# Optimization experiments

Measured on AMD Instinct MI355X. Metric: run time of the kernel, lower is better.

The kernel has to match this reference:

```python
import jax, jax.numpy as jnp
import numpy as np

N_HEADS = 8
D_K = 256
SCALE = D_K ** -0.5


def setup_inputs() -> dict:
    key = jax.random.key(0)
    k1, k2, k3 = jax.random.split(key, 3)
    B, C, H, W = 8, 256, 32, 32
    x = jax.random.normal(k1, (B, C, H, W), dtype=jnp.float32)
    Wp = jax.random.normal(k2, (C, N_HEADS * D_K * 3), dtype=jnp.float32) * (C ** -0.5)
    bp = jnp.zeros((N_HEADS * D_K * 3,), dtype=jnp.float32)
    Wo = jax.random.normal(k3, (N_HEADS * D_K, C), dtype=jnp.float32) * ((N_HEADS * D_K) ** -0.5)
    bo = jnp.zeros((C,), dtype=jnp.float32)
    return {"x": x, "Wp": Wp, "bp": bp, "Wo": Wo, "bo": bo}


def reference(x, Wp, bp, Wo, bo):
    B, C, H, W = x.shape
    S = H * W
    # [B,C,H,W] -> [B,S,C] tokens
    xt = x.reshape(B, C, S).transpose(0, 2, 1)
    qkv = (xt @ Wp + bp).reshape(B, S, N_HEADS, 3 * D_K)
    q, k, v = jnp.split(qkv, 3, axis=-1)  # each [B,S,H,dk]
    attn = jnp.einsum('bihd,bjhd->bijh', q, k) * SCALE
    attn = jax.nn.softmax(attn, axis=2)  # over j (keys)
    res = jnp.einsum('bijh,bjhd->bihd', attn, v).reshape(B, S, N_HEADS * D_K)
    res = res @ Wo + bo + xt  # residual
    return res.transpose(0, 2, 1).reshape(B, C, H, W)
```

## Files before the change

kernel.cpp:

```cpp
#include <hip/hip_runtime.h>

#define NH    8
#define DK    256
#define SS    1024
#define QSCALE 0.09016844136947155f
#define TSH   8192

using frag8  = __attribute__((ext_vector_type(8))) short;
using f32x16 = __attribute__((ext_vector_type(16))) float;

__device__ __forceinline__ unsigned short f2bf(float f) {
    unsigned int u = __float_as_uint(f);
    return (unsigned short)((u + 0x7FFFu + ((u >> 16) & 1u)) >> 16);
}
__device__ __forceinline__ unsigned int pk2bf(float lo, float hi) {
    unsigned int ul = __float_as_uint(lo), uh = __float_as_uint(hi);
    ul += 0x7FFFu + ((ul >> 16) & 1u);
    uh += 0x7FFFu + ((uh >> 16) & 1u);
    return (ul >> 16) | (uh & 0xFFFF0000u);
}

__device__ __forceinline__ void load_lds16(const void* g, void* l) {
    __builtin_amdgcn_global_load_lds(
        (const __attribute__((address_space(1))) unsigned int*)g,
        (__attribute__((address_space(3))) unsigned int*)l, 16, 0, 0);
}


__global__ __launch_bounds__(256) void k0_all(
    const float* __restrict__ x,  unsigned short* __restrict__ xbT,
    const float* __restrict__ Wp, unsigned short* __restrict__ WptT,
    const float* __restrict__ Wo, unsigned short* __restrict__ WotT)
{
    __shared__ float tile[32][33];
    const int bid = blockIdx.x;
    const float* in; unsigned short* outp; int C, c0, r0; size_t pbase; int psz;
    if (bid < 2048) {
        int rr = bid;
        int b = rr >> 8;
        in = x + (size_t)b * 256 * 1024;
        C = 1024; c0 = (rr & 31) * 32; r0 = ((rr >> 5) & 7) * 32;
        psz = 8192; pbase = (size_t)(b * 32 + (c0 >> 5)); outp = xbT;
    } else if (bid < 3584) {
        int rr = bid - 2048;
        in = Wp; C = 6144; c0 = (rr % 192) * 32; r0 = (rr / 192) * 32;
        psz = 8192; pbase = (size_t)(c0 >> 5); outp = WptT;
    } else {
        int rr = bid - 3584;
        in = Wo; C = 256; c0 = (rr & 7) * 32; r0 = (rr >> 3) * 32;
        psz = 65536; pbase = (size_t)(c0 >> 5); outp = WotT;
    }
    const int tx = threadIdx.x & 31, ty = threadIdx.x >> 5;
#pragma unroll
    for (int j = 0; j < 4; j++)
        tile[ty + j * 8][tx] = in[(size_t)(r0 + ty + j * 8) * C + c0 + tx];
    __syncthreads();
    const int k = r0 + tx;
    unsigned short* dst = outp + pbase * psz + ((k >> 3) * 32) * 8 + (k & 7);
#pragma unroll
    for (int j = 0; j < 4; j++)
        dst[(ty + j * 8) * 8] = f2bf(tile[tx][ty + j * 8]);
}

__global__ __launch_bounds__(256) void k1_qkv(
    const unsigned short* __restrict__ xbT, const unsigned short* __restrict__ WptT,
    const float* __restrict__ bp,
    unsigned short* __restrict__ qb, unsigned short* __restrict__ kb,
    unsigned short* __restrict__ vb)
{
    __shared__ unsigned short Xs[2][4096];
    __shared__ unsigned short Ws[2][4096];
    const int t = threadIdx.x;
    const int wave = t >> 6, lane = t & 63;
    const int l32 = lane & 31, hw = lane >> 5;
    const int n0 = blockIdx.x * 128, m0 = blockIdx.y * 128;
    const int b = m0 >> 10, s0 = m0 & 1023;

    const int h = n0 / 768;
    const int rem = n0 - h * 768;
    const int tt = rem >> 8;
    const int dcol0 = rem & 255;

    const unsigned short* Xg = xbT + (size_t)(b * 32 + (s0 >> 5)) * TSH;
    const unsigned short* Wg = WptT + (size_t)(n0 >> 5) * TSH;

    f32x16 acc[4];
#pragma unroll
    for (int j = 0; j < 4; j++)
#pragma unroll
        for (int r = 0; r < 16; r++) acc[j][r] = 0.f;

    auto stage = [&](int buf, int kt) {
#pragma unroll
        for (int j = 0; j < 4; j++) {
            int rgn = wave * 4 + j;
            if (rgn < 8) {
                int p = rgn >> 1, half = rgn & 1;
                load_lds16(Xg + (size_t)p * TSH + kt * 1024 + half * 512 + lane * 8,
                           &Xs[buf][p * 1024 + half * 512]);
            } else {
                int r2 = rgn - 8, p = r2 >> 1, half = r2 & 1;
                load_lds16(Wg + (size_t)p * TSH + kt * 1024 + half * 512 + lane * 8,
                           &Ws[buf][p * 1024 + half * 512]);
            }
        }
    };

    stage(0, 0);
    __syncthreads();

    for (int kt = 0; kt < 8; kt++) {
        const int cur = kt & 1;
        if (kt < 7) stage(cur ^ 1, kt + 1);
        const unsigned short* Fa = (tt < 2) ? &Ws[cur][wave * 1024] : &Xs[cur][wave * 1024];
        const unsigned short* Fb = (tt < 2) ? &Xs[cur][0] : &Ws[cur][0];
#pragma unroll
        for (int t2 = 0; t2 < 2; t2++) {
            frag8 af = *(const frag8*)(Fa + (2 * t2 + hw) * 256 + l32 * 8);
#pragma unroll
            for (int j = 0; j < 4; j++) {
                frag8 bf = *(const frag8*)(Fb + j * 1024 + (2 * t2 + hw) * 256 + l32 * 8);
                acc[j] = __builtin_amdgcn_mfma_f32_32x32x16_bf16(af, bf, acc[j], 0, 0, 0);
            }
        }
        __syncthreads();
    }

    if (tt < 2) {
        const float sc = (tt == 0) ? QSCALE : 1.0f;
        unsigned short* dst0 = (tt == 0 ? qb : kb);
        const int dc0 = (dcol0 + wave * 32) >> 3;
#pragma unroll
        for (int G = 0; G < 4; G++) {
            float4 bb = *(const float4*)(&bp[n0 + wave * 32 + 4 * hw + 8 * G]);
#pragma unroll
            for (int j = 0; j < 4; j++) {
                unsigned short* cell = dst0
                    + (size_t)((b * NH + h) * 32 + (s0 >> 5) + j) * TSH
                    + ((dc0 + G) * 32 + l32) * 8 + 4 * hw;
                uint2 st;
                st.x = pk2bf((acc[j][4 * G + 0] + bb.x) * sc, (acc[j][4 * G + 1] + bb.y) * sc);
                st.y = pk2bf((acc[j][4 * G + 2] + bb.z) * sc, (acc[j][4 * G + 3] + bb.w) * sc);
                *(uint2*)cell = st;
            }
        }
    } else {
        unsigned short* vt = vb + (size_t)((b * NH + h) * 32 + (s0 >> 5) + wave) * TSH;
#pragma unroll
        for (int j = 0; j < 4; j++) {
            const int d = dcol0 + j * 32 + l32;
            const float bv = bp[n0 + j * 32 + l32];
#pragma unroll
            for (int G = 0; G < 4; G++) {
                int g = G >> 1;
                unsigned short* cell = vt + (g * 2 + hw) * 2048 + d * 8 + 4 * (G & 1);
                uint2 st;
                st.x = pk2bf(acc[j][4 * G + 0] + bv, acc[j][4 * G + 1] + bv);
                st.y = pk2bf(acc[j][4 * G + 2] + bv, acc[j][4 * G + 3] + bv);
                *(uint2*)cell = st;
            }
        }
    }
}

__global__ __launch_bounds__(256, 2) void k2_attn(
    const unsigned short* __restrict__ qb, const unsigned short* __restrict__ kb,
    const unsigned short* __restrict__ vb, unsigned short* __restrict__ ob)
{
    __shared__ unsigned short Ks[2][TSH];
    __shared__ unsigned short Vs[2][TSH];

    const int t = threadIdx.x;
    const int wave = t >> 6, lane = t & 63;
    const int l32 = lane & 31, hw = lane >> 5;

    const int flat = blockIdx.x;
    const int xcd = flat & 7, tt2 = flat >> 3;
    const int qt = tt2 & 7;
    const int bh = xcd * 8 + (tt2 >> 3);

    frag8 qf[16];
    {
        const unsigned short* qp = qb + ((size_t)bh * 32 + qt * 4 + wave) * TSH
                                 + hw * 256 + l32 * 8;
#pragma unroll
        for (int s = 0; s < 16; s++) qf[s] = *(const frag8*)(qp + s * 512);
    }

    f32x16 acc[8];
#pragma unroll
    for (int nb = 0; nb < 8; nb++)
#pragma unroll
        for (int r = 0; r < 16; r++) acc[nb][r] = 0.f;
    float lsum = 0.f;

    const unsigned short* kt0 = kb + (size_t)bh * 32 * TSH;
    const unsigned short* vt0 = vb + (size_t)bh * 32 * TSH;

#pragma unroll
    for (int j = 0; j < 4; j++) {
        int c = wave * 4 + j;
        load_lds16(kt0 + c * 512 + lane * 8, &Ks[0][c * 512]);
        load_lds16(vt0 + c * 512 + lane * 8, &Vs[0][c * 512]);
    }
    __syncthreads();

    for (int kt = 0; kt < 32; kt++) {
        const int cur = kt & 1;

        if (kt < 31) {
            const unsigned short* kg = kt0 + (size_t)(kt + 1) * TSH;
            const unsigned short* vg = vt0 + (size_t)(kt + 1) * TSH;
#pragma unroll
            for (int j = 0; j < 4; j++) {
                int c = wave * 4 + j;
                load_lds16(kg + c * 512 + lane * 8, &Ks[cur ^ 1][c * 512]);
                load_lds16(vg + c * 512 + lane * 8, &Vs[cur ^ 1][c * 512]);
            }
        }

        f32x16 sa0, sa1;
#pragma unroll
        for (int r = 0; r < 16; r++) { sa0[r] = 0.f; sa1[r] = 0.f; }
#pragma unroll
        for (int s = 0; s < 16; s += 2) {
            frag8 kf0 = *(const frag8*)(&Ks[cur][(2 * s + hw) * 256 + l32 * 8]);
            frag8 kf1 = *(const frag8*)(&Ks[cur][(2 * s + 2 + hw) * 256 + l32 * 8]);
            sa0 = __builtin_amdgcn_mfma_f32_32x32x16_bf16(kf0, qf[s], sa0, 0, 0, 0);
            sa1 = __builtin_amdgcn_mfma_f32_32x32x16_bf16(kf1, qf[s + 1], sa1, 0, 0, 0);
        }

        float p[16];
#pragma unroll
        for (int e = 0; e < 16; e++) {
            p[e] = exp2f(sa0[e] + sa1[e]);
            lsum += p[e];
        }
        frag8 pf[2];
#pragma unroll
        for (int g = 0; g < 2; g++) {
            uint4 w;
            w.x = pk2bf(p[g * 8 + 0], p[g * 8 + 1]);
            w.y = pk2bf(p[g * 8 + 2], p[g * 8 + 3]);
            w.z = pk2bf(p[g * 8 + 4], p[g * 8 + 5]);
            w.w = pk2bf(p[g * 8 + 6], p[g * 8 + 7]);
            pf[g] = *(frag8*)&w;
        }

#pragma unroll
        for (int g = 0; g < 2; g++)
#pragma unroll
            for (int nb = 0; nb < 8; nb++) {
                frag8 vf = *(const frag8*)(&Vs[cur][(g * 2 + hw) * 2048 + (nb * 32 + l32) * 8]);
                acc[nb] = __builtin_amdgcn_mfma_f32_32x32x16_bf16(vf, pf[g], acc[nb], 0, 0, 0);
            }

        __syncthreads();
    }

    lsum += __shfl_xor(lsum, 32);
    const float li = 1.f / lsum;

    unsigned short* opan = ob + ((size_t)bh * 32 + qt * 4 + wave) * TSH;
#pragma unroll
    for (int nb = 0; nb < 8; nb++)
#pragma unroll
        for (int G = 0; G < 4; G++) {
            unsigned short* cell = opan + ((nb * 4 + G) * 32 + l32) * 8 + 4 * hw;
            uint2 st;
            st.x = pk2bf(acc[nb][4 * G + 0] * li, acc[nb][4 * G + 1] * li);
            st.y = pk2bf(acc[nb][4 * G + 2] * li, acc[nb][4 * G + 3] * li);
            *(uint2*)cell = st;
        }
}

__global__ __launch_bounds__(256) void k3_proj(
    const unsigned short* __restrict__ Ob, const unsigned short* __restrict__ WotT,
    const float* __restrict__ bo, const float* __restrict__ x,
    float* __restrict__ out)
{
    __shared__ unsigned short As[2][2048];
    __shared__ unsigned short Bs[2][4096];
    const int t = threadIdx.x;
    const int wave = t >> 6, lane = t & 63;
    const int l32 = lane & 31, hw = lane >> 5;
    const int wc = wave & 1, wt = wave >> 1;
    const int c0 = blockIdx.x * 64, m0 = blockIdx.y * 128;
    const int b = m0 >> 10, s0 = m0 & 1023;

    const unsigned short* Ag = WotT + (size_t)(c0 >> 5) * 65536;

    f32x16 acc[2];
#pragma unroll
    for (int pp = 0; pp < 2; pp++)
#pragma unroll
        for (int r = 0; r < 16; r++) acc[pp][r] = 0.f;

    auto stage = [&](int buf, int kt) {
        const int hh = kt >> 3, lc = (kt & 7) * 4;
#pragma unroll
        for (int j = 0; j < 3; j++) {
            int rgn = wave * 3 + j;
            if (rgn < 4) {
                int wp = rgn >> 1, half = rgn & 1;
                load_lds16(Ag + (size_t)wp * 65536 + kt * 1024 + half * 512 + lane * 8,
                           &As[buf][wp * 1024 + half * 512]);
            } else {
                int r2 = rgn - 4, p = r2 >> 1, half = r2 & 1;
                load_lds16(Ob + (size_t)((b * NH + hh) * 32 + (s0 >> 5) + p) * TSH
                               + lc * 256 + half * 512 + lane * 8,
                           &Bs[buf][p * 1024 + half * 512]);
            }
        }
    };

    stage(0, 0);
    __syncthreads();

    for (int kt = 0; kt < 64; kt++) {
        const int cur = kt & 1;
        if (kt < 63) stage(cur ^ 1, kt + 1);
#pragma unroll
        for (int t2 = 0; t2 < 2; t2++) {
            frag8 af = *(const frag8*)(&As[cur][wc * 1024 + (2 * t2 + hw) * 256 + l32 * 8]);
#pragma unroll
            for (int pp = 0; pp < 2; pp++) {
                frag8 bf = *(const frag8*)(&Bs[cur][(wt * 2 + pp) * 1024 + (2 * t2 + hw) * 256 + l32 * 8]);
                acc[pp] = __builtin_amdgcn_mfma_f32_32x32x16_bf16(af, bf, acc[pp], 0, 0, 0);
            }
        }
        __syncthreads();
    }

#pragma unroll
    for (int G = 0; G < 4; G++) {
        float4 bb = *(const float4*)(&bo[c0 + wc * 32 + 4 * hw + 8 * G]);
#pragma unroll
        for (int pp = 0; pp < 2; pp++) {
            const int s = s0 + wt * 64 + pp * 32 + l32;
#pragma unroll
            for (int e = 0; e < 4; e++) {
                const int ch = c0 + wc * 32 + 4 * hw + 8 * G + e;
                const float bbe = (e == 0) ? bb.x : (e == 1) ? bb.y : (e == 2) ? bb.z : bb.w;
                size_t off = (size_t)(b * 256 + ch) * 1024 + s;
                out[off] = acc[pp][4 * G + e] + bbe + x[off];
            }
        }
    }
}

extern "C" void kernel_launch(void* const* d_in, const int* in_sizes, int n_in,
                              void* d_out, int out_size, void* d_ws, size_t ws_size,
                              hipStream_t stream)
{
    const float* x  = (const float*)d_in[0];
    const float* Wp = (const float*)d_in[1];
    const float* bp = (const float*)d_in[2];
    const float* Wo = (const float*)d_in[3];
    const float* bo = (const float*)d_in[4];
    float* out = (float*)d_out;

    char* ws = (char*)d_ws;
    unsigned short* qb   = (unsigned short*)(ws);
    unsigned short* kb   = (unsigned short*)(ws + 33554432);
    unsigned short* vb   = (unsigned short*)(ws + 67108864);
    unsigned short* xbT  = (unsigned short*)(ws + 100663296);
    unsigned short* WptT = (unsigned short*)(ws + 104857600);
    unsigned short* WotT = (unsigned short*)(ws + 108003328);

    k0_all<<<dim3(4096), 256, 0, stream>>>(x, xbT, Wp, WptT, Wo, WotT);
    k1_qkv<<<dim3(48, 64), 256, 0, stream>>>(xbT, WptT, bp, qb, kb, vb);
    k2_attn<<<dim3(512), 256, 0, stream>>>(qb, kb, vb, qb );
    k3_proj<<<dim3(4, 64), 256, 0, stream>>>(qb, WotT, bo, x, out);
}
```

Baseline: 225.3 us.

## Enlarge QKV and projection GEMM tiles and unroll double-buffer loops statically

The QKV GEMM now computes 256x128 tiles per block (8 accumulators per wave), which halves the grid and raises reuse of the weight tile. The attention and QKV main loops are unrolled by two so LDS buffer indices become compile-time constants, removing dynamic buffer selection. The output projection moves to 512-thread blocks with a K-step of 64, giving each wave one accumulator and half as many loop iterations and barriers. In exchange, register pressure in the QKV kernel and LDS use per block go up, and the smaller QKV grid means fewer blocks to spread across CUs.

After: 229.6 us. About the same (+1.9%).

```diff
diff --git a/kernel.cpp b/kernel.cpp
--- a/kernel.cpp
+++ b/kernel.cpp
@@ -68,12 +68,13 @@
     unsigned short* __restrict__ qb, unsigned short* __restrict__ kb,
     unsigned short* __restrict__ vb)
 {
-    __shared__ unsigned short Xs[2][4096];
+    __shared__ unsigned short Xs[2][8192];
     __shared__ unsigned short Ws[2][4096];
     const int t = threadIdx.x;
     const int wave = t >> 6, lane = t & 63;
     const int l32 = lane & 31, hw = lane >> 5;
-    const int n0 = blockIdx.x * 128, m0 = blockIdx.y * 128;
+    const int n0 = blockIdx.x * 128;
+    const int m0 = blockIdx.y * 256;
     const int b = m0 >> 10, s0 = m0 & 1023;
 
     const int h = n0 / 768;
@@ -84,47 +85,65 @@
     const unsigned short* Xg = xbT + (size_t)(b * 32 + (s0 >> 5)) * TSH;
     const unsigned short* Wg = WptT + (size_t)(n0 >> 5) * TSH;
 
-    f32x16 acc[4];
-#pragma unroll
-    for (int j = 0; j < 4; j++)
+    f32x16 acc[8];
+#pragma unroll
+    for (int j = 0; j < 8; j++)
 #pragma unroll
         for (int r = 0; r < 16; r++) acc[j][r] = 0.f;
 
     auto stage = [&](int buf, int kt) {
 #pragma unroll
-        for (int j = 0; j < 4; j++) {
-            int rgn = wave * 4 + j;
-            if (rgn < 8) {
+        for (int j = 0; j < 6; j++) {
+            int rgn = wave * 6 + j;
+            if (rgn < 16) {
                 int p = rgn >> 1, half = rgn & 1;
                 load_lds16(Xg + (size_t)p * TSH + kt * 1024 + half * 512 + lane * 8,
                            &Xs[buf][p * 1024 + half * 512]);
             } else {
-                int r2 = rgn - 8, p = r2 >> 1, half = r2 & 1;
+                int r2 = rgn - 16, p = r2 >> 1, half = r2 & 1;
                 load_lds16(Wg + (size_t)p * TSH + kt * 1024 + half * 512 + lane * 8,
                            &Ws[buf][p * 1024 + half * 512]);
             }
         }
     };
 
+    auto body = [&](const unsigned short* Xb, const unsigned short* Wb) {
+        if (tt < 2) {
+#pragma unroll
+            for (int t2 = 0; t2 < 2; t2++) {
+                frag8 af = *(const frag8*)(Wb + wave * 1024 + (2 * t2 + hw) * 256 + l32 * 8);
+#pragma unroll
+                for (int j = 0; j < 8; j++) {
+                    frag8 bf = *(const frag8*)(Xb + j * 1024 + (2 * t2 + hw) * 256 + l32 * 8);
+                    acc[j] = __builtin_amdgcn_mfma_f32_32x32x16_bf16(af, bf, acc[j], 0, 0, 0);
+                }
+            }
+        } else {
+#pragma unroll
+            for (int t2 = 0; t2 < 2; t2++) {
+                frag8 bfv[4];
+#pragma unroll
+                for (int j = 0; j < 4; j++)
+                    bfv[j] = *(const frag8*)(Wb + j * 1024 + (2 * t2 + hw) * 256 + l32 * 8);
+#pragma unroll
+                for (int mi = 0; mi < 2; mi++) {
+                    frag8 af = *(const frag8*)(Xb + (wave * 2 + mi) * 1024 + (2 * t2 + hw) * 256 + l32 * 8);
+#pragma unroll
+                    for (int j = 0; j < 4; j++)
+                        acc[mi * 4 + j] = __builtin_amdgcn_mfma_f32_32x32x16_bf16(af, bfv[j], acc[mi * 4 + j], 0, 0, 0);
+                }
+            }
+        }
+    };
+
     stage(0, 0);
     __syncthreads();
-
-    for (int kt = 0; kt < 8; kt++) {
-        const int cur = kt & 1;
-        if (kt < 7) stage(cur ^ 1, kt + 1);
-        const unsigned short* Fa = (tt < 2) ? &Ws[cur][wave * 1024] : &Xs[cur][wave * 1024];
-        const unsigned short* Fb = (tt < 2) ? &Xs[cur][0] : &Ws[cur][0];
-#pragma unroll
-        for (int t2 = 0; t2 < 2; t2++) {
-            frag8 af = *(const frag8*)(Fa + (2 * t2 + hw) * 256 + l32 * 8);
-#pragma unroll
-            for (int j = 0; j < 4; j++) {
-                frag8 bf = *(const frag8*)(Fb + j * 1024 + (2 * t2 + hw) * 256 + l32 * 8);
-                acc[j] = __builtin_amdgcn_mfma_f32_32x32x16_bf16(af, bf, acc[j], 0, 0, 0);
-            }
-        }
-        __syncthreads();
-    }
+    for (int kt = 0; kt < 6; kt += 2) {
+        stage(1, kt + 1); body(&Xs[0][0], &Ws[0][0]); __syncthreads();
+        stage(0, kt + 2); body(&Xs[1][0], &Ws[1][0]); __syncthreads();
+    }
+    stage(1, 7); body(&Xs[0][0], &Ws[0][0]); __syncthreads();
+    body(&Xs[1][0], &Ws[1][0]);
 
     if (tt < 2) {
         const float sc = (tt == 0) ? QSCALE : 1.0f;
@@ -134,7 +153,7 @@
         for (int G = 0; G < 4; G++) {
             float4 bb = *(const float4*)(&bp[n0 + wave * 32 + 4 * hw + 8 * G]);
 #pragma unroll
-            for (int j = 0; j < 4; j++) {
+            for (int j = 0; j < 8; j++) {
                 unsigned short* cell = dst0
                     + (size_t)((b * NH + h) * 32 + (s0 >> 5) + j) * TSH
                     + ((dc0 + G) * 32 + l32) * 8 + 4 * hw;
@@ -145,19 +164,23 @@
             }
         }
     } else {
-        unsigned short* vt = vb + (size_t)((b * NH + h) * 32 + (s0 >> 5) + wave) * TSH;
-#pragma unroll
-        for (int j = 0; j < 4; j++) {
-            const int d = dcol0 + j * 32 + l32;
-            const float bv = bp[n0 + j * 32 + l32];
-#pragma unroll
-            for (int G = 0; G < 4; G++) {
-                int g = G >> 1;
-                unsigned short* cell = vt + (g * 2 + hw) * 2048 + d * 8 + 4 * (G & 1);
-                uint2 st;
-                st.x = pk2bf(acc[j][4 * G + 0] + bv, acc[j][4 * G + 1] + bv);
-                st.y = pk2bf(acc[j][4 * G + 2] + bv, acc[j][4 * G + 3] + bv);
-                *(uint2*)cell = st;
+        unsigned short* vt0 = vb + (size_t)((b * NH + h) * 32 + (s0 >> 5)) * TSH;
+#pragma unroll
+        for (int mi = 0; mi < 2; mi++) {
+            unsigned short* vt = vt0 + (size_t)(wave * 2 + mi) * TSH;
+#pragma unroll
+            for (int j = 0; j < 4; j++) {
+                const int d = dcol0 + j * 32 + l32;
+                const float bv = bp[n0 + j * 32 + l32];
+#pragma unroll
+                for (int G = 0; G < 4; G++) {
+                    int g = G >> 1;
+                    unsigned short* cell = vt + (g * 2 + hw) * 2048 + d * 8 + 4 * (G & 1);
+                    uint2 st;
+                    st.x = pk2bf(acc[mi * 4 + j][4 * G + 0] + bv, acc[mi * 4 + j][4 * G + 1] + bv);
+                    st.y = pk2bf(acc[mi * 4 + j][4 * G + 2] + bv, acc[mi * 4 + j][4 * G + 3] + bv);
+                    *(uint2*)cell = st;
+                }
             }
         }
     }
@@ -194,42 +217,28 @@
         for (int r = 0; r < 16; r++) acc[nb][r] = 0.f;
     float lsum = 0.f;
 
-    const unsigned short* kt0 = kb + (size_t)bh * 32 * TSH;
-    const unsigned short* vt0 = vb + (size_t)bh * 32 * TSH;
-
-#pragma unroll
-    for (int j = 0; j < 4; j++) {
-        int c = wave * 4 + j;
-        load_lds16(kt0 + c * 512 + lane * 8, &Ks[0][c * 512]);
-        load_lds16(vt0 + c * 512 + lane * 8, &Vs[0][c * 512]);
-    }
-    __syncthreads();
-
-    for (int kt = 0; kt < 32; kt++) {
-        const int cur = kt & 1;
-
-        if (kt < 31) {
-            const unsigned short* kg = kt0 + (size_t)(kt + 1) * TSH;
-            const unsigned short* vg = vt0 + (size_t)(kt + 1) * TSH;
-#pragma unroll
-            for (int j = 0; j < 4; j++) {
-                int c = wave * 4 + j;
-                load_lds16(kg + c * 512 + lane * 8, &Ks[cur ^ 1][c * 512]);
-                load_lds16(vg + c * 512 + lane * 8, &Vs[cur ^ 1][c * 512]);
-            }
-        }
-
+    const unsigned short* kstg = kb + (size_t)bh * 32 * TSH + wave * 2048 + lane * 8;
+    const unsigned short* vstg = vb + (size_t)bh * 32 * TSH + wave * 2048 + lane * 8;
+
+    auto prefetch = [&](int buf, int kt) {
+#pragma unroll
+        for (int j = 0; j < 4; j++) {
+            load_lds16(kstg + (size_t)kt * TSH + j * 512, &Ks[buf][wave * 2048 + j * 512]);
+            load_lds16(vstg + (size_t)kt * TSH + j * 512, &Vs[buf][wave * 2048 + j * 512]);
+        }
+    };
+
+    auto body = [&](const unsigned short* Kb, const unsigned short* Vb) {
         f32x16 sa0, sa1;
 #pragma unroll
         for (int r = 0; r < 16; r++) { sa0[r] = 0.f; sa1[r] = 0.f; }
 #pragma unroll
         for (int s = 0; s < 16; s += 2) {
-            frag8 kf0 = *(const frag8*)(&Ks[cur][(2 * s + hw) * 256 + l32 * 8]);
-            frag8 kf1 = *(const frag8*)(&Ks[cur][(2 * s + 2 + hw) * 256 + l32 * 8]);
+            frag8 kf0 = *(const frag8*)(Kb + (2 * s + hw) * 256 + l32 * 8);
+            frag8 kf1 = *(const frag8*)(Kb + (2 * s + 2 + hw) * 256 + l32 * 8);
             sa0 = __builtin_amdgcn_mfma_f32_32x32x16_bf16(kf0, qf[s], sa0, 0, 0, 0);
             sa1 = __builtin_amdgcn_mfma_f32_32x32x16_bf16(kf1, qf[s + 1], sa1, 0, 0, 0);
         }
-
         float p[16];
 #pragma unroll
         for (int e = 0; e < 16; e++) {
@@ -246,17 +255,29 @@
             w.w = pk2bf(p[g * 8 + 6], p[g * 8 + 7]);
             pf[g] = *(frag8*)&w;
         }
-
 #pragma unroll
         for (int g = 0; g < 2; g++)
 #pragma unroll
             for (int nb = 0; nb < 8; nb++) {
-                frag8 vf = *(const frag8*)(&Vs[cur][(g * 2 + hw) * 2048 + (nb * 32 + l32) * 8]);
+                frag8 vf = *(const frag8*)(Vb + (g * 2 + hw) * 2048 + (nb * 32 + l32) * 8);
                 acc[nb] = __builtin_amdgcn_mfma_f32_32x32x16_bf16(vf, pf[g], acc[nb], 0, 0, 0);
             }
-
+    };
+
+    prefetch(0, 0);
+    __syncthreads();
+    for (int kt = 0; kt < 30; kt += 2) {
+        prefetch(1, kt + 1);
+        body(&Ks[0][0], &Vs[0][0]);
         __syncthreads();
-    }
+        prefetch(0, kt + 2);
+        body(&Ks[1][0], &Vs[1][0]);
+        __syncthreads();
+    }
+    prefetch(1, 31);
+    body(&Ks[0][0], &Vs[0][0]);
+    __syncthreads();
+    body(&Ks[1][0], &Vs[1][0]);
 
     lsum += __shfl_xor(lsum, 32);
     const float li = 1.f / lsum;
@@ -274,13 +295,13 @@
         }
 }
 
-__global__ __launch_bounds__(256) void k3_proj(
+__global__ __launch_bounds__(512) void k3_proj(
     const unsigned short* __restrict__ Ob, const unsigned short* __restrict__ WotT,
     const float* __restrict__ bo, const float* __restrict__ x,
     float* __restrict__ out)
 {
-    __shared__ unsigned short As[2][2048];
-    __shared__ unsigned short Bs[2][4096];
+    __shared__ unsigned short As[2][4096];
+    __shared__ unsigned short Bs[2][8192];
     const int t = threadIdx.x;
     const int wave = t >> 6, lane = t & 63;
     const int l32 = lane & 31, hw = lane >> 5;
@@ -290,61 +311,56 @@
 
     const unsigned short* Ag = WotT + (size_t)(c0 >> 5) * 65536;
 
-    f32x16 acc[2];
-#pragma unroll
-    for (int pp = 0; pp < 2; pp++)
-#pragma unroll
-        for (int r = 0; r < 16; r++) acc[pp][r] = 0.f;
+    f32x16 acc;
+#pragma unroll
+    for (int r = 0; r < 16; r++) acc[r] = 0.f;
 
     auto stage = [&](int buf, int kt) {
-        const int hh = kt >> 3, lc = (kt & 7) * 4;
+        const int hh = kt >> 2, lc = (kt & 3) * 8;
 #pragma unroll
         for (int j = 0; j < 3; j++) {
             int rgn = wave * 3 + j;
-            if (rgn < 4) {
-                int wp = rgn >> 1, half = rgn & 1;
-                load_lds16(Ag + (size_t)wp * 65536 + kt * 1024 + half * 512 + lane * 8,
-                           &As[buf][wp * 1024 + half * 512]);
+            if (rgn < 8) {
+                int wp = rgn >> 2, q4 = rgn & 3;
+                load_lds16(Ag + (size_t)wp * 65536 + kt * 2048 + q4 * 512 + lane * 8,
+                           &As[buf][wp * 2048 + q4 * 512]);
             } else {
-                int r2 = rgn - 4, p = r2 >> 1, half = r2 & 1;
+                int r2 = rgn - 8, p = r2 >> 2, q4 = r2 & 3;
                 load_lds16(Ob + (size_t)((b * NH + hh) * 32 + (s0 >> 5) + p) * TSH
-                               + lc * 256 + half * 512 + lane * 8,
-                           &Bs[buf][p * 1024 + half * 512]);
-            }
+                               + lc * 256 + q4 * 512 + lane * 8,
+                           &Bs[buf][p * 2048 + q4 * 512]);
+            }
+        }
+    };
+
+    auto body = [&](const unsigned short* Ab, const unsigned short* Bb) {
+#pragma unroll
+        for (int t2 = 0; t2 < 4; t2++) {
+            frag8 af = *(const frag8*)(Ab + wc * 2048 + (2 * t2 + hw) * 256 + l32 * 8);
+            frag8 bf = *(const frag8*)(Bb + wt * 2048 + (2 * t2 + hw) * 256 + l32 * 8);
+            acc = __builtin_amdgcn_mfma_f32_32x32x16_bf16(af, bf, acc, 0, 0, 0);
         }
     };
 
     stage(0, 0);
     __syncthreads();
-
-    for (int kt = 0; kt < 64; kt++) {
-        const int cur = kt & 1;
-        if (kt < 63) stage(cur ^ 1, kt + 1);
-#pragma unroll
-        for (int t2 = 0; t2 < 2; t2++) {
-            frag8 af = *(const frag8*)(&As[cur][wc * 1024 + (2 * t2 + hw) * 256 + l32 * 8]);
-#pragma unroll
-            for (int pp = 0; pp < 2; pp++) {
-                frag8 bf = *(const frag8*)(&Bs[cur][(wt * 2 + pp) * 1024 + (2 * t2 + hw) * 256 + l32 * 8]);
-                acc[pp] = __builtin_amdgcn_mfma_f32_32x32x16_bf16(af, bf, acc[pp], 0, 0, 0);
-            }
-        }
-        __syncthreads();
-    }
-
+    for (int kt = 0; kt < 30; kt += 2) {
+        stage(1, kt + 1); body(&As[0][0], &Bs[0][0]); __syncthreads();
+        stage(0, kt + 2); body(&As[1][0], &Bs[1][0]); __syncthreads();
+    }
+    stage(1, 31); body(&As[0][0], &Bs[0][0]); __syncthreads();
+    body(&As[1][0], &Bs[1][0]);
+
+    const int s = s0 + wt * 32 + l32;
 #pragma unroll
     for (int G = 0; G < 4; G++) {
         float4 bb = *(const float4*)(&bo[c0 + wc * 32 + 4 * hw + 8 * G]);
 #pragma unroll
-        for (int pp = 0; pp < 2; pp++) {
-            const int s = s0 + wt * 64 + pp * 32 + l32;
-#pragma unroll
-            for (int e = 0; e < 4; e++) {
-                const int ch = c0 + wc * 32 + 4 * hw + 8 * G + e;
-                const float bbe = (e == 0) ? bb.x : (e == 1) ? bb.y : (e == 2) ? bb.z : bb.w;
-                size_t off = (size_t)(b * 256 + ch) * 1024 + s;
-                out[off] = acc[pp][4 * G + e] + bbe + x[off];
-            }
+        for (int e = 0; e < 4; e++) {
+            const int ch = c0 + wc * 32 + 4 * hw + 8 * G + e;
+            const float bbe = (e == 0) ? bb.x : (e == 1) ? bb.y : (e == 2) ? bb.z : bb.w;
+            size_t off = (size_t)(b * 256 + ch) * 1024 + s;
+            out[off] = acc[4 * G + e] + bbe + x[off];
         }
     }
 }
@@ -369,7 +385,7 @@
     unsigned short* WotT = (unsigned short*)(ws + 108003328);
 
     k0_all<<<dim3(4096), 256, 0, stream>>>(x, xbT, Wp, WptT, Wo, WotT);
-    k1_qkv<<<dim3(48, 64), 256, 0, stream>>>(xbT, WptT, bp, qb, kb, vb);
+    k1_qkv<<<dim3(48, 32), 256, 0, stream>>>(xbT, WptT, bp, qb, kb, vb);
     k2_attn<<<dim3(512), 256, 0, stream>>>(qb, kb, vb, qb );
-    k3_proj<<<dim3(4, 64), 256, 0, stream>>>(qb, WotT, bo, x, out);
-}
+    k3_proj<<<dim3(4, 64), 512, 0, stream>>>(qb, WotT, bo, x, out);
+}
```
